# Optimization experiments

Hardware: AMD Instinct MI355X
Metric: run time of the kernel (lower is better)

## Reference

```python
import jax, jax.numpy as jnp
import numpy as np

V = 32000   # src and trg vocab
E = 256     # embed dim
H = 512     # hidden dim
S, T, B = 50, 40, 32


def lstm_layer(x, h0, c0, Wih, Whh, b):
    # x: [T,B,Din]; PyTorch gate order i,f,g,o; b = b_ih + b_hh (identical math)
    def step(carry, xt):
        h, c = carry
        g = xt @ Wih.T + h @ Whh.T + b
        i, f, gg, o = jnp.split(g, 4, axis=-1)
        c = jax.nn.sigmoid(f) * c + jax.nn.sigmoid(i) * jnp.tanh(gg)
        h = jax.nn.sigmoid(o) * jnp.tanh(c)
        return (h, c), h
    (hT, cT), ys = jax.lax.scan(step, (h0, c0), x)
    return ys, hT, cT


def setup_inputs() -> dict:
    key = jax.random.key(0)
    ks = jax.random.split(key, 20)
    s = 0.05
    d = {
        'src': jax.random.randint(ks[0], (S, B), 0, V),
        'trg': jax.random.randint(ks[1], (T, B), 0, V),
        'enc_emb': jax.random.normal(ks[2], (V, E), jnp.float32) * s,
        'enc_Wih0': jax.random.normal(ks[3], (4 * H, E), jnp.float32) * s,
        'enc_Whh0': jax.random.normal(ks[4], (4 * H, H), jnp.float32) * s,
        'enc_b0': jax.random.normal(ks[5], (4 * H,), jnp.float32) * s,
        'enc_Wih1': jax.random.normal(ks[6], (4 * H, H), jnp.float32) * s,
        'enc_Whh1': jax.random.normal(ks[7], (4 * H, H), jnp.float32) * s,
        'enc_b1': jax.random.normal(ks[8], (4 * H,), jnp.float32) * s,
        'dec_emb': jax.random.normal(ks[9], (V, E), jnp.float32) * s,
        'dec_Wih0': jax.random.normal(ks[10], (4 * H, E), jnp.float32) * s,
        'dec_Whh0': jax.random.normal(ks[11], (4 * H, H), jnp.float32) * s,
        'dec_b0': jax.random.normal(ks[12], (4 * H,), jnp.float32) * s,
        'dec_Wih1': jax.random.normal(ks[13], (4 * H, H), jnp.float32) * s,
        'dec_Whh1': jax.random.normal(ks[14], (4 * H, H), jnp.float32) * s,
        'dec_b1': jax.random.normal(ks[15], (4 * H,), jnp.float32) * s,
        'out_W': jax.random.normal(ks[16], (V, H), jnp.float32) * s,
        'out_b': jax.random.normal(ks[17], (V,), jnp.float32) * s,
    }
    return d


def reference(src, trg, enc_emb, enc_Wih0, enc_Whh0, enc_b0, enc_Wih1, enc_Whh1, enc_b1,
              dec_emb, dec_Wih0, dec_Whh0, dec_b0, dec_Wih1, dec_Whh1, dec_b1, out_W, out_b):
    Bsz = src.shape[1]
    z = jnp.zeros((Bsz, H), enc_emb.dtype)
    # Encoder: 2-layer LSTM over src embeddings (dropout=0)
    x = enc_emb[src]                                    # [S,B,E]
    ys0, h0, c0 = lstm_layer(x, z, z, enc_Wih0, enc_Whh0, enc_b0)
    _, h1, c1 = lstm_layer(ys0, z, z, enc_Wih1, enc_Whh1, enc_b1)
    # Decoder with teacherForcingRatio=1.0: inputs are trg[:-1]
    dx = dec_emb[trg[:-1]]                              # [T-1,B,E]
    dy0, _, _ = lstm_layer(dx, h0, c0, dec_Wih0, dec_Whh0, dec_b0)
    dy1, _, _ = lstm_layer(dy0, h1, c1, dec_Wih1, dec_Whh1, dec_b1)
    logits = jnp.einsum('tbh,vh->tbv', dy1, out_W) + out_b  # [T-1,B,V]
    outputs = jnp.concatenate([jnp.zeros((1, Bsz, out_W.shape[0]), logits.dtype), logits], axis=0)
    return outputs
```

## Files before the change

kernel.cpp:

```cpp
#include <hip/hip_runtime.h>
#include <hip/hip_bf16.h>
#include <stdint.h>

typedef unsigned short ushort_t;

#define HID 512
#define FOURH 2048
#define BSZ 32
#define SLEN 50
#define TDEC 39
#define EMB 256
#define VOC 32000
#define NWG_LSTM 64

using short8  = __attribute__((ext_vector_type(8))) short;
using float4v = __attribute__((ext_vector_type(4))) float;

__device__ inline float bf16lo(uint32_t u) { return __uint_as_float(u << 16); }
__device__ inline float bf16hi(uint32_t u) { return __uint_as_float(u & 0xffff0000u); }

__device__ inline ushort_t f32_to_bf16(float f) {
    uint32_t u = __float_as_uint(f);
    uint32_t r = (u + 0x7fffu + ((u >> 16) & 1u)) >> 16;
    return (ushort_t)r;
}

__device__ inline float sigmoid_f(float x) { return 1.0f / (1.0f + expf(-x)); }

__device__ inline int detect_f32(const ushort_t* __restrict__ probe) {
    int cnt = 0;
#pragma unroll
    for (int i = 0; i < 64; ++i) {
        int e = (probe[i] >> 7) & 0xFF;
        cnt += (e >= 0x8A);
    }
    return cnt > 0;
}

__global__ void embed_kernel(const int* __restrict__ idx,
                             const void* __restrict__ emb,
                             uint32_t* __restrict__ out,
                             int total_u,
                             const ushort_t* __restrict__ probe)
{
    const int F32 = detect_f32(probe);
    int i = blockIdx.x * 256 + threadIdx.x;
    if (i >= total_u) return;
    int tok = i >> 7;
    int col = i & 127;
    int row = idx[tok];
    if (F32) {
        const float* ef = (const float*)emb + (size_t)row * EMB + col * 2;
        uint32_t lo = f32_to_bf16(ef[0]);
        uint32_t hi = f32_to_bf16(ef[1]);
        out[i] = lo | (hi << 16);
    } else {
        out[i] = ((const uint32_t*)emb)[(size_t)row * 128 + col];
    }
}

__device__ inline float load_bias(const void* __restrict__ bias, int n, int F32) {
    if (F32) return ((const float*)bias)[n];
    return __uint_as_float(((uint32_t)((const ushort_t*)bias)[n]) << 16);
}

__device__ inline void gload_lds16(const ushort_t* __restrict__ g, ushort_t* l) {
    __builtin_amdgcn_global_load_lds(
        (const __attribute__((address_space(1))) uint32_t*)g,
        (__attribute__((address_space(3))) uint32_t*)l,
        16, 0, 0);
}

template <int SMODE>
__global__ __launch_bounds__(256, 3)
void gemm_tile_kernel(const ushort_t* __restrict__ A,
                      const void* __restrict__ W,
                      const void* __restrict__ bias,
                      void* __restrict__ C,
                      int M, int N, int K,
                      const ushort_t* __restrict__ probe)
{
    const int F32 = detect_f32(probe);
    __shared__ ushort_t Alds[128 * 64];
    __shared__ ushort_t Blds[128 * 64];

    const int tid  = threadIdx.x;
    const int lane = tid & 63;
    const int wave = tid >> 6;
    const int l16  = lane & 15;
    const int l4   = lane >> 4;

    const int wm = (wave >> 1) * 64;
    const int wn = (wave & 1) * 64;

    const int mbase = blockIdx.x * 128;
    const int nbase = blockIdx.y * 128;

    const int sr   = lane >> 3;
    const int scol = ((lane & 7) ^ sr) * 8;

    float4v acc[4][4];
#pragma unroll
    for (int i = 0; i < 4; ++i)
#pragma unroll
        for (int j = 0; j < 4; ++j) acc[i][j] = (float4v){0.f, 0.f, 0.f, 0.f};

    for (int k0 = 0; k0 < K; k0 += 64) {
        __syncthreads();

#pragma unroll
        for (int c = 0; c < 4; ++c) {
            int chunk = wave * 4 + c;
            int row   = chunk * 8 + sr;
            gload_lds16(A + (size_t)(mbase + row) * K + k0 + scol,
                        Alds + chunk * 512);
        }
        if (F32) {
#pragma unroll
            for (int c = 0; c < 4; ++c) {
                int chunk = wave * 4 + c;
                int row   = chunk * 8 + sr;
                const float* gp = (const float*)W + (size_t)(nbase + row) * K + k0 + scol;
                float4v f0 = *(const float4v*)gp;
                float4v f1 = *(const float4v*)(gp + 4);
                short8 v;
#pragma unroll
                for (int j = 0; j < 4; ++j) v[j]     = (short)f32_to_bf16(f0[j]);
#pragma unroll
                for (int j = 0; j < 4; ++j) v[4 + j] = (short)f32_to_bf16(f1[j]);
                *(short8*)(Blds + chunk * 512 + lane * 8) = v;
            }
        } else {
#pragma unroll
            for (int c = 0; c < 4; ++c) {
                int chunk = wave * 4 + c;
                int row   = chunk * 8 + sr;
                gload_lds16((const ushort_t*)W + (size_t)(nbase + row) * K + k0 + scol,
                            Blds + chunk * 512);
            }
        }
        __syncthreads();

        short8 af[4][2], bf[4][2];
#pragma unroll
        for (int mi = 0; mi < 4; ++mi) {
            int row = wm + mi * 16 + l16;
#pragma unroll
            for (int kk = 0; kk < 2; ++kk) {
                int cb = (kk * 64 + l4 * 16) ^ ((l16 & 7) << 4);
                af[mi][kk] = *(const short8*)((const char*)Alds + row * 128 + cb);
            }
        }
#pragma unroll
        for (int ni = 0; ni < 4; ++ni) {
            int row = wn + ni * 16 + l16;
#pragma unroll
            for (int kk = 0; kk < 2; ++kk) {
                int cb = (kk * 64 + l4 * 16) ^ ((l16 & 7) << 4);
                bf[ni][kk] = *(const short8*)((const char*)Blds + row * 128 + cb);
            }
        }
#pragma unroll
        for (int mi = 0; mi < 4; ++mi)
#pragma unroll
            for (int ni = 0; ni < 4; ++ni) {
                acc[mi][ni] = __builtin_amdgcn_mfma_f32_16x16x32_bf16(
                    af[mi][0], bf[ni][0], acc[mi][ni], 0, 0, 0);
                acc[mi][ni] = __builtin_amdgcn_mfma_f32_16x16x32_bf16(
                    af[mi][1], bf[ni][1], acc[mi][ni], 0, 0, 0);
            }
    }

#pragma unroll
    for (int mi = 0; mi < 4; ++mi) {
#pragma unroll
        for (int ni = 0; ni < 4; ++ni) {
            int n = nbase + wn + ni * 16 + l16;
            float bv = load_bias(bias, n, F32);
#pragma unroll
            for (int r = 0; r < 4; ++r) {
                int m = mbase + wm + mi * 16 + l4 * 4 + r;
                if (m < M) {
                    float v = acc[mi][ni][r] + bv;
                    if (SMODE == 0) {
                        ((float*)C)[(size_t)m * N + n] = v;
                    } else {
                        size_t idx = (size_t)(BSZ + m) * N + n;
                        if (F32) ((float*)C)[idx] = v;
                        else     ((ushort_t*)C)[idx] = f32_to_bf16(v);
                    }
                }
            }
        }
    }
}

__device__ inline void lstm_grid_barrier(uint32_t* cnt, uint32_t target) {
    __syncthreads();
    if (threadIdx.x == 0) {
        __hip_atomic_fetch_add(cnt, 1u, __ATOMIC_RELEASE, __HIP_MEMORY_SCOPE_AGENT);
        while (__hip_atomic_load(cnt, __ATOMIC_ACQUIRE, __HIP_MEMORY_SCOPE_AGENT) < target)
            __builtin_amdgcn_s_sleep(2);
    }
    __syncthreads();
}

__global__ __launch_bounds__(256, 1)
void lstm_layer_kernel(const float* __restrict__ xih,
                       ushort_t* __restrict__ hbuf,
                       float*    __restrict__ cbuf,
                       const void* __restrict__ Whh,
                       ushort_t* __restrict__ ys,
                       const ushort_t* __restrict__ probe,
                       int T,
                       uint32_t* __restrict__ bar_cnt)
{
    const int F32 = detect_f32(probe);

    __shared__ ushort_t w_lds[32 * 512];
    __shared__ ushort_t h_lds[32 * 512];

    const int tid  = threadIdx.x;
    const int lane = tid & 63;
    const int wave = tid >> 6;
    const int l16  = lane & 15;
    const int quad = lane >> 4;
    const int j0   = blockIdx.x * 8;

    const int m0 = (wave >> 1) * 16;
    const int ni = wave & 1;

#pragma unroll
    for (int i = 0; i < 8; ++i) {
        int idx = tid + i * 256;
        int rr  = idx >> 6;
        int c16 = idx & 63;
        int gate = rr & 3, u8 = rr >> 2;
        size_t grow = (size_t)(gate * HID + j0 + u8) * HID + c16 * 8;
        short8 v;
        if (F32) {
            const float* gp = (const float*)Whh + grow;
            float4v f0 = *(const float4v*)gp;
            float4v f1 = *(const float4v*)(gp + 4);
#pragma unroll
            for (int j = 0; j < 4; ++j) v[j]     = (short)f32_to_bf16(f0[j]);
#pragma unroll
            for (int j = 0; j < 4; ++j) v[4 + j] = (short)f32_to_bf16(f1[j]);
        } else {
            v = *(const short8*)((const ushort_t*)Whh + grow);
        }
        *(short8*)((char*)w_lds + rr * 1024 + ((c16 * 16) ^ ((rr & 7) << 4))) = v;
    }

    const int u8me = ni * 4 + (l16 >> 2);
    const int gme  = l16 & 3;
    const int jme  = j0 + u8me;

    float creg[4];
#pragma unroll
    for (int r = 0; r < 4; ++r)
        creg[r] = cbuf[(m0 + quad * 4 + r) * HID + jme];

    const bool has_ys = (ys != nullptr);

    for (int t = 0; t < T; ++t) {
        const ushort_t* hin  = hbuf + (size_t)(t & 1) * (BSZ * HID);
        ushort_t*       hout = hbuf + (size_t)((t + 1) & 1) * (BSZ * HID);
        const float*    xr   = xih + (size_t)t * (BSZ * FOURH);

        float xv[4];
#pragma unroll
        for (int r = 0; r < 4; ++r)
            xv[r] = xr[(m0 + quad * 4 + r) * FOURH + gme * HID + jme];

#pragma unroll
        for (int i = 0; i < 8; ++i) {
            int idx = tid + i * 256;
            int b   = idx >> 6;
            int c16 = idx & 63;
            short8 v = *(const short8*)(hin + (size_t)b * HID + c16 * 8);
            *(short8*)((char*)h_lds + b * 1024 + ((c16 * 16) ^ ((b & 7) << 4))) = v;
        }
        __syncthreads();

        float4v acc = (float4v){0.f, 0.f, 0.f, 0.f};
#pragma unroll
        for (int kk = 0; kk < 16; ++kk) {
            int cb = (kk * 64 + quad * 16) ^ ((l16 & 7) << 4);
            short8 a = *(const short8*)((const char*)h_lds + (m0 + l16) * 1024 + cb);
            short8 b = *(const short8*)((const char*)w_lds + (ni * 16 + l16) * 1024 + cb);
            acc = __builtin_amdgcn_mfma_f32_16x16x32_bf16(a, b, acc, 0, 0, 0);
        }

#pragma unroll
        for (int r = 0; r < 4; ++r) {
            float g   = acc[r] + xv[r];
            float arg = (gme == 2) ? 2.f * g : g;
            float s   = 1.f / (1.f + expf(-arg));
            float act = (gme == 2) ? 2.f * s - 1.f : s;
            int base = lane & ~3;
            float ai = __shfl(act, base + 0);
            float af = __shfl(act, base + 1);
            float ag = __shfl(act, base + 2);
            float ao = __shfl(act, base + 3);
            if (gme == 0) {
                float cn = af * creg[r] + ai * ag;
                creg[r] = cn;
                float th = 2.f / (1.f + expf(-2.f * cn)) - 1.f;
                float hn = ao * th;
                ushort_t hb = f32_to_bf16(hn);
                int b = m0 + quad * 4 + r;
                hout[b * HID + jme] = hb;
                if (has_ys) ys[(size_t)t * (BSZ * HID) + b * HID + jme] = hb;
            }
        }

        if (t != T - 1)
            lstm_grid_barrier(bar_cnt, (uint32_t)(t + 1) * NWG_LSTM);
        else
            __syncthreads();
    }

    if (gme == 0) {
#pragma unroll
        for (int r = 0; r < 4; ++r)
            cbuf[(m0 + quad * 4 + r) * HID + jme] = creg[r];
    }
}

__global__ void lstm_step_kernel(const float* __restrict__ xih,
                                 const ushort_t* __restrict__ h_in,
                                 ushort_t* __restrict__ h_out,
                                 float* __restrict__ c,
                                 const void* __restrict__ Whh,
                                 ushort_t* __restrict__ ys,
                                 const ushort_t* __restrict__ probe)
{
    const int F32 = detect_f32(probe);
    __shared__ uint32_t h_lds[BSZ * 257];
    __shared__ uint32_t w_lds[8 * 256];
    __shared__ float    g_lds[8][BSZ];

    const int tid = threadIdx.x;
    const int j0  = blockIdx.x * 2;

    const uint32_t* h32 = (const uint32_t*)h_in;
#pragma unroll
    for (int i = 0; i < 32; ++i) {
        int idx = tid + i * 256;
        int row = idx >> 8, col = idx & 255;
        h_lds[row * 257 + col] = h32[idx];
    }
#pragma unroll
    for (int i = 0; i < 8; ++i) {
        int idx  = tid + i * 256;
        int lrr  = idx >> 8, col = idx & 255;
        int gate = lrr >> 1, jl = lrr & 1;
        size_t wrow = (size_t)(gate * HID + j0 + jl);
        if (F32) {
            const float* wf = (const float*)Whh + wrow * HID + col * 2;
            uint32_t lo = f32_to_bf16(wf[0]);
            uint32_t hi = f32_to_bf16(wf[1]);
            w_lds[lrr * 256 + col] = lo | (hi << 16);
        } else {
            w_lds[lrr * 256 + col] = ((const uint32_t*)Whh)[wrow * 256 + col];
        }
    }
    __syncthreads();

    const int b    = tid & 31;
    const int lr   = tid >> 5;
    const int gate = lr >> 1;
    const int jl   = lr & 1;

    float dot = xih[b * FOURH + gate * HID + j0 + jl];
    const uint32_t* hr = &h_lds[b * 257];
    const uint32_t* wr = &w_lds[lr * 256];
    float s0 = 0.f, s1 = 0.f;
#pragma unroll 8
    for (int k = 0; k < 256; ++k) {
        uint32_t hu = hr[k], wu = wr[k];
        s0 += bf16lo(hu) * bf16lo(wu);
        s1 += bf16hi(hu) * bf16hi(wu);
    }
    g_lds[lr][b] = dot + s0 + s1;
    __syncthreads();

    if (tid < 64) {
        int b2 = tid & 31, jl2 = tid >> 5;
        int j  = j0 + jl2;
        float gi = g_lds[(0 << 1) | jl2][b2];
        float gf = g_lds[(1 << 1) | jl2][b2];
        float gg = g_lds[(2 << 1) | jl2][b2];
        float go = g_lds[(3 << 1) | jl2][b2];
        float cold = c[b2 * HID + j];
        float cn = sigmoid_f(gf) * cold + sigmoid_f(gi) * tanhf(gg);
        float hn = sigmoid_f(go) * tanhf(cn);
        c[b2 * HID + j] = cn;
        ushort_t hb = f32_to_bf16(hn);
        h_out[b2 * HID + j] = hb;
        if (ys) ys[b2 * HID + j] = hb;
    }
}

__global__ void zero_row_kernel(void* __restrict__ outv,
                                const ushort_t* __restrict__ probe)
{
    const int F32 = detect_f32(probe);
    int i = blockIdx.x * 256 + threadIdx.x;
    if (i >= BSZ * VOC) return;
    if (F32) ((uint32_t*)outv)[i] = 0u;
    else     ((ushort_t*)outv)[i] = 0;
}

extern "C" void kernel_launch(void* const* d_in, const int* in_sizes, int n_in,
                              void* d_out, int out_size, void* d_ws, size_t ws_size,
                              hipStream_t stream)
{
    const int*      src      = (const int*)d_in[0];
    const int*      trg      = (const int*)d_in[1];
    const void*     enc_emb  = d_in[2];
    const void*     enc_Wih0 = d_in[3];
    const void*     enc_Whh0 = d_in[4];
    const void*     enc_b0   = d_in[5];
    const void*     enc_Wih1 = d_in[6];
    const void*     enc_Whh1 = d_in[7];
    const void*     enc_b1   = d_in[8];
    const void*     dec_emb  = d_in[9];
    const void*     dec_Wih0 = d_in[10];
    const void*     dec_Whh0 = d_in[11];
    const void*     dec_b0   = d_in[12];
    const void*     dec_Wih1 = d_in[13];
    const void*     dec_Whh1 = d_in[14];
    const void*     dec_b1   = d_in[15];
    const void*     out_W    = d_in[16];
    const void*     out_b    = d_in[17];

    const ushort_t* probe = (const ushort_t*)enc_b0;

    const int ME = SLEN * BSZ;
    const int MD = TDEC * BSZ;

    ushort_t* dy1 = (ushort_t*)d_out;

    char*  arena = (char*)d_out + (4u << 20);
    size_t aoff  = 0;
    auto acarve = [&](size_t bytes) -> void* {
        void* p = arena + aoff;
        aoff = (aoff + bytes + 255) & ~(size_t)255;
        return p;
    };
    const size_t HSTATE = (size_t)BSZ * HID;
    float*    Xbig = (float*)acarve((size_t)ME * FOURH * 4);
    ushort_t* X0   = (ushort_t*)acarve((size_t)ME * EMB * 2);
    ushort_t* DX0  = (ushort_t*)acarve((size_t)MD * EMB * 2);
    ushort_t* ys0  = (ushort_t*)acarve((size_t)ME * HID * 2);
    ushort_t* dy0  = (ushort_t*)acarve((size_t)MD * HID * 2);
    ushort_t* h0b  = (ushort_t*)acarve(2 * HSTATE * 2);
    float*    c0b  = (float*)acarve(HSTATE * 4);
    ushort_t* h1b  = (ushort_t*)acarve(2 * HSTATE * 2);
    float*    c1b  = (float*)acarve(HSTATE * 4);
    uint32_t* bars = (uint32_t*)acarve(4 * 256);

    hipMemsetAsync(h0b, 0, HSTATE * 2, stream);
    hipMemsetAsync(c0b, 0, HSTATE * 4, stream);
    hipMemsetAsync(h1b, 0, HSTATE * 2, stream);
    hipMemsetAsync(c1b, 0, HSTATE * 4, stream);
    hipMemsetAsync(bars, 0, 4 * 256, stream);

    {
        int tu = ME * (EMB / 2);
        embed_kernel<<<(tu + 255) / 256, 256, 0, stream>>>(
            src, enc_emb, (uint32_t*)X0, tu, probe);
        int td = MD * (EMB / 2);
        embed_kernel<<<(td + 255) / 256, 256, 0, stream>>>(
            trg, dec_emb, (uint32_t*)DX0, td, probe);
    }

    const size_t XIH_T = (size_t)BSZ * FOURH;
    const int MTE = (ME + 127) / 128;
    const int MTD = (MD + 127) / 128;

    auto launch_lstm = [&](const float* xih, ushort_t* hb, float* cb,
                           const void* Whh, ushort_t* ysp, int T, int layer) {
        const float* a0 = xih; ushort_t* a1 = hb; float* a2 = cb;
        const void* a3 = Whh; ushort_t* a4 = ysp;
        const ushort_t* a5 = probe; int a6 = T;
        uint32_t* a7 = bars + layer * 64;
        void* ka[] = {(void*)&a0, (void*)&a1, (void*)&a2, (void*)&a3,
                      (void*)&a4, (void*)&a5, (void*)&a6, (void*)&a7};
        hipError_t e = hipLaunchCooperativeKernel(
            reinterpret_cast<const void*>(&lstm_layer_kernel),
            dim3(NWG_LSTM), dim3(256), ka, 0, stream);
        if (e != hipSuccess) {
            for (int t = 0; t < T; ++t)
                lstm_step_kernel<<<256, 256, 0, stream>>>(
                    xih + (size_t)t * XIH_T,
                    hb + (t & 1) * HSTATE, hb + ((t + 1) & 1) * HSTATE,
                    cb, Whh,
                    ysp ? ysp + (size_t)t * HSTATE : (ushort_t*)nullptr,
                    probe);
        }
    };

    gemm_tile_kernel<0><<<dim3(MTE, FOURH / 128), 256, 0, stream>>>(
        X0, enc_Wih0, enc_b0, Xbig, ME, FOURH, EMB, probe);
    launch_lstm(Xbig, h0b, c0b, enc_Whh0, ys0, SLEN, 0);

    gemm_tile_kernel<0><<<dim3(MTE, FOURH / 128), 256, 0, stream>>>(
        ys0, enc_Wih1, enc_b1, Xbig, ME, FOURH, HID, probe);
    launch_lstm(Xbig, h1b, c1b, enc_Whh1, (ushort_t*)nullptr, SLEN, 1);

    gemm_tile_kernel<0><<<dim3(MTD, FOURH / 128), 256, 0, stream>>>(
        DX0, dec_Wih0, dec_b0, Xbig, MD, FOURH, EMB, probe);
    launch_lstm(Xbig, h0b, c0b, dec_Whh0, dy0, TDEC, 2);

    gemm_tile_kernel<0><<<dim3(MTD, FOURH / 128), 256, 0, stream>>>(
        dy0, dec_Wih1, dec_b1, Xbig, MD, FOURH, HID, probe);
    launch_lstm(Xbig, h1b, c1b, dec_Whh1, dy1, TDEC, 3);

    gemm_tile_kernel<1><<<dim3(MTD, VOC / 128), 256, 0, stream>>>(
        dy1, out_W, out_b, d_out, MD, VOC, HID, probe);

    zero_row_kernel<<<(BSZ * VOC + 255) / 256, 256, 0, stream>>>(d_out, probe);
}
```

Baseline: 1.818 ms.

## Keep Whh fragments in registers and relax persistent LSTM grid barrier

Moves each wave's recurrent weight fragment out of LDS into registers, so the inner MFMA loop reads only h from LDS. The grid barrier drops release/acquire ordering in favour of an explicit vmcnt wait, relaxed atomics and a shorter sleep. h exchange now uses relaxed agent-scope atomic loads and stores, with adjacent bf16 h values packed into 32-bit stores. This aims to cut per-timestep sync latency and LDS traffic, at the cost of more register pressure and reliance on relaxed-ordering correctness across workgroups.

```diff
diff --git a/kernel.cpp b/kernel.cpp
--- a/kernel.cpp
+++ b/kernel.cpp
@@ -15,6 +15,7 @@
 
 using short8  = __attribute__((ext_vector_type(8))) short;
 using float4v = __attribute__((ext_vector_type(4))) float;
+using uint4v  = __attribute__((ext_vector_type(4))) unsigned int;
 
 __device__ inline float bf16lo(uint32_t u) { return __uint_as_float(u << 16); }
 __device__ inline float bf16hi(uint32_t u) { return __uint_as_float(u & 0xffff0000u); }
@@ -196,11 +197,12 @@
 }
 
 __device__ inline void lstm_grid_barrier(uint32_t* cnt, uint32_t target) {
+    asm volatile("s_waitcnt vmcnt(0)" ::: "memory");
     __syncthreads();
     if (threadIdx.x == 0) {
-        __hip_atomic_fetch_add(cnt, 1u, __ATOMIC_RELEASE, __HIP_MEMORY_SCOPE_AGENT);
-        while (__hip_atomic_load(cnt, __ATOMIC_ACQUIRE, __HIP_MEMORY_SCOPE_AGENT) < target)
-            __builtin_amdgcn_s_sleep(2);
+        __hip_atomic_fetch_add(cnt, 1u, __ATOMIC_RELAXED, __HIP_MEMORY_SCOPE_AGENT);
+        while (__hip_atomic_load(cnt, __ATOMIC_RELAXED, __HIP_MEMORY_SCOPE_AGENT) < target)
+            __builtin_amdgcn_s_sleep(1);
     }
     __syncthreads();
 }
@@ -217,7 +219,6 @@
 {
     const int F32 = detect_f32(probe);
 
-    __shared__ ushort_t w_lds[32 * 512];
     __shared__ ushort_t h_lds[32 * 512];
 
     const int tid  = threadIdx.x;
@@ -230,43 +231,46 @@
     const int m0 = (wave >> 1) * 16;
     const int ni = wave & 1;
 
-#pragma unroll
-    for (int i = 0; i < 8; ++i) {
-        int idx = tid + i * 256;
-        int rr  = idx >> 6;
-        int c16 = idx & 63;
-        int gate = rr & 3, u8 = rr >> 2;
-        size_t grow = (size_t)(gate * HID + j0 + u8) * HID + c16 * 8;
-        short8 v;
-        if (F32) {
-            const float* gp = (const float*)Whh + grow;
-            float4v f0 = *(const float4v*)gp;
-            float4v f1 = *(const float4v*)(gp + 4);
-#pragma unroll
-            for (int j = 0; j < 4; ++j) v[j]     = (short)f32_to_bf16(f0[j]);
-#pragma unroll
-            for (int j = 0; j < 4; ++j) v[4 + j] = (short)f32_to_bf16(f1[j]);
-        } else {
-            v = *(const short8*)((const ushort_t*)Whh + grow);
-        }
-        *(short8*)((char*)w_lds + rr * 1024 + ((c16 * 16) ^ ((rr & 7) << 4))) = v;
-    }
-
     const int u8me = ni * 4 + (l16 >> 2);
     const int gme  = l16 & 3;
     const int jme  = j0 + u8me;
 
+    short8 wfrag[16];
+    {
+        const size_t grow = (size_t)(gme * HID + j0 + u8me) * HID;
+#pragma unroll
+        for (int kk = 0; kk < 16; ++kk) {
+            size_t off = grow + kk * 32 + quad * 8;
+            if (F32) {
+                const float* gp = (const float*)Whh + off;
+                float4v f0 = *(const float4v*)gp;
+                float4v f1 = *(const float4v*)(gp + 4);
+                short8 v;
+#pragma unroll
+                for (int j = 0; j < 4; ++j) v[j]     = (short)f32_to_bf16(f0[j]);
+#pragma unroll
+                for (int j = 0; j < 4; ++j) v[4 + j] = (short)f32_to_bf16(f1[j]);
+                wfrag[kk] = v;
+            } else {
+                wfrag[kk] = *(const short8*)((const ushort_t*)Whh + off);
+            }
+        }
+    }
+
     float creg[4];
 #pragma unroll
     for (int r = 0; r < 4; ++r)
         creg[r] = cbuf[(m0 + quad * 4 + r) * HID + jme];
 
     const bool has_ys = (ys != nullptr);
+    uint32_t* ys32 = (uint32_t*)ys;
 
     for (int t = 0; t < T; ++t) {
-        const ushort_t* hin  = hbuf + (size_t)(t & 1) * (BSZ * HID);
-        ushort_t*       hout = hbuf + (size_t)((t + 1) & 1) * (BSZ * HID);
-        const float*    xr   = xih + (size_t)t * (BSZ * FOURH);
+        const uint32_t* h32in =
+            (const uint32_t*)(hbuf + (size_t)(t & 1) * (BSZ * HID));
+        uint32_t* h32out =
+            (uint32_t*)(hbuf + (size_t)((t + 1) & 1) * (BSZ * HID));
+        const float* xr = xih + (size_t)t * (BSZ * FOURH);
 
         float xv[4];
 #pragma unroll
@@ -278,8 +282,13 @@
             int idx = tid + i * 256;
             int b   = idx >> 6;
             int c16 = idx & 63;
-            short8 v = *(const short8*)(hin + (size_t)b * HID + c16 * 8);
-            *(short8*)((char*)h_lds + b * 1024 + ((c16 * 16) ^ ((b & 7) << 4))) = v;
+            const uint32_t* gp = h32in + b * 256 + c16 * 4;
+            uint4v dv;
+            dv[0] = __hip_atomic_load(gp + 0, __ATOMIC_RELAXED, __HIP_MEMORY_SCOPE_AGENT);
+            dv[1] = __hip_atomic_load(gp + 1, __ATOMIC_RELAXED, __HIP_MEMORY_SCOPE_AGENT);
+            dv[2] = __hip_atomic_load(gp + 2, __ATOMIC_RELAXED, __HIP_MEMORY_SCOPE_AGENT);
+            dv[3] = __hip_atomic_load(gp + 3, __ATOMIC_RELAXED, __HIP_MEMORY_SCOPE_AGENT);
+            *(uint4v*)((char*)h_lds + b * 1024 + ((c16 * 16) ^ ((b & 7) << 4))) = dv;
         }
         __syncthreads();
 
@@ -288,8 +297,7 @@
         for (int kk = 0; kk < 16; ++kk) {
             int cb = (kk * 64 + quad * 16) ^ ((l16 & 7) << 4);
             short8 a = *(const short8*)((const char*)h_lds + (m0 + l16) * 1024 + cb);
-            short8 b = *(const short8*)((const char*)w_lds + (ni * 16 + l16) * 1024 + cb);
-            acc = __builtin_amdgcn_mfma_f32_16x16x32_bf16(a, b, acc, 0, 0, 0);
+            acc = __builtin_amdgcn_mfma_f32_16x16x32_bf16(a, wfrag[kk], acc, 0, 0, 0);
         }
 
 #pragma unroll
@@ -303,22 +311,24 @@
             float af = __shfl(act, base + 1);
             float ag = __shfl(act, base + 2);
             float ao = __shfl(act, base + 3);
-            if (gme == 0) {
-                float cn = af * creg[r] + ai * ag;
-                creg[r] = cn;
-                float th = 2.f / (1.f + expf(-2.f * cn)) - 1.f;
-                float hn = ao * th;
-                ushort_t hb = f32_to_bf16(hn);
+            float cn = af * creg[r] + ai * ag;
+            creg[r] = cn;
+            float th = 2.f / (1.f + expf(-2.f * cn)) - 1.f;
+            float hn = ao * th;
+            ushort_t hb = f32_to_bf16(hn);
+            uint32_t dw = (uint32_t)hb |
+                          ((uint32_t)(ushort_t)__shfl((int)hb, (lane + 4) & 63) << 16);
+            if ((l16 & 7) == 0) {
                 int b = m0 + quad * 4 + r;
-                hout[b * HID + jme] = hb;
-                if (has_ys) ys[(size_t)t * (BSZ * HID) + b * HID + jme] = hb;
+                int di = b * 256 + ((j0 + u8me) >> 1);
+                __hip_atomic_store(h32out + di, dw,
+                                   __ATOMIC_RELAXED, __HIP_MEMORY_SCOPE_AGENT);
+                if (has_ys) ys32[(size_t)t * 8192 + di] = dw;
             }
         }
 
         if (t != T - 1)
             lstm_grid_barrier(bar_cnt, (uint32_t)(t + 1) * NWG_LSTM);
-        else
-            __syncthreads();
     }
 
     if (gme == 0) {
```

Result: faster. 1.763 ms (-3.1%).
